# Kernel tuning notes

Measured on AMD Instinct MI355X. Metric: run time of the kernel, lower is better.

The kernel has to match this reference:

```python
import jax, jax.numpy as jnp
import numpy as np

N = 16      # manifold_dim
H = 128     # hidden_dim
B = 256     # batch
EPS = 1e-6


def setup_inputs() -> dict:
    key = jax.random.key(0)
    ks = jax.random.split(key, 14)
    def w(k, shape):
        fan_in = shape[0]
        return jax.random.uniform(k, shape, jnp.float32, -1.0, 1.0) / np.sqrt(fan_in)
    return {
        "points": jax.random.normal(ks[0], (B, N), jnp.float32),
        # metric network: N -> H -> N*N
        "mW1": w(ks[1], (N, H)), "mb1": jnp.zeros((H,), jnp.float32),
        "mW2": w(ks[2], (H, N * N)), "mb2": jnp.zeros((N * N,), jnp.float32),
        # christoffel network: 3 -> H -> 1
        "cW1": w(ks[3], (3, H)), "cb1": jnp.zeros((H,), jnp.float32),
        "cW2": w(ks[4], (H, 1)), "cb2": jnp.zeros((1,), jnp.float32),
        # ricci network: 4N -> 2H -> N*N
        "rW1": w(ks[5], (4 * N, 2 * H)), "rb1": jnp.zeros((2 * H,), jnp.float32),
        "rW2": w(ks[6], (2 * H, N * N)), "rb2": jnp.zeros((N * N,), jnp.float32),
    }


def reference(points, mW1, mb1, mW2, mb2, cW1, cb1, cW2, cb2, rW1, rb1, rW2, rb2):
    b = points.shape[0]
    n = N
    # ---- metric: (b, n, n) ----
    mh = jax.nn.relu(points @ mW1 + mb1)
    metric = (mh @ mW2 + mb2).reshape(b, n, n)
    metric = metric + EPS * jnp.eye(n, dtype=metric.dtype)
    metric = 0.5 * (metric + jnp.swapaxes(metric, -2, -1))

    # ---- christoffel: vectorized over all (i,j,k) triples ----
    # inputs per triple: [metric_ij, metric_jk, metric_ki]
    m_ij = jnp.broadcast_to(metric[:, :, :, None], (b, n, n, n))
    m_jk = jnp.broadcast_to(metric[:, None, :, :], (b, n, n, n))
    mT = jnp.swapaxes(metric, -2, -1)  # mT[b,i,k] = metric[b,k,i]
    m_ki = jnp.broadcast_to(mT[:, :, None, :], (b, n, n, n))
    ch_in = jnp.stack([m_ij, m_jk, m_ki], axis=-1)        # (b,n,n,n,3)
    ch_h = jnp.tanh(ch_in @ cW1 + cb1)                    # (b,n,n,n,H)
    christoffel = (ch_h @ cW2 + cb2)[..., 0]              # (b,n,n,n)

    # ---- ricci: vectorized over all (i,j) pairs ----
    p_b = jnp.broadcast_to(points[:, None, None, :], (b, n, n, n))
    m_i = jnp.broadcast_to(metric[:, :, None, :], (b, n, n, n))
    m_j = jnp.broadcast_to(metric[:, None, :, :], (b, n, n, n))
    r_in = jnp.concatenate([p_b, m_i, m_j, christoffel], axis=-1)  # (b,n,n,4n)
    r_h = jax.nn.relu(r_in @ rW1 + rb1)                   # (b,n,n,2H)
    r_out = (r_h @ rW2 + rb2).reshape(b, n, n, n, n)      # (b,i,j,n,n)
    r_out = 0.5 * (r_out + jnp.swapaxes(r_out, -1, -2))
    ricci = r_out.sum(axis=(1, 2)) / (n * n)              # (b,n,n)
    return ricci
```

## Files before the change

kernel.cpp:

```cpp
#include <hip/hip_runtime.h>
#include <hip/hip_bf16.h>

#define NDIM 16
#define HDIM 128
#define BATCH 256
#define EPS_D 1e-6f

typedef float v2f __attribute__((ext_vector_type(2)));
static __device__ __forceinline__ v2f v2(float a, float b) {
  v2f r; r.x = a; r.y = b; return r;
}
static __device__ __forceinline__ v2f splat(float a) {
  v2f r; r.x = a; r.y = a; return r;
}

__global__ __launch_bounds__(256) void metric_proj_kernel(
    const float* __restrict__ points,
    const float* __restrict__ mW1, const float* __restrict__ mb1,
    const float* __restrict__ mW2, const float* __restrict__ mb2,
    const float* __restrict__ rW1, const float* __restrict__ rb1,
    float* __restrict__ metric,
    float* __restrict__ A1, float* __restrict__ Mi, float* __restrict__ Mj,
    float* __restrict__ G) {
  int b = blockIdx.x;
  int t = threadIdx.x;
  __shared__ float p[16];
  __shared__ float mh[128];
  __shared__ float raw[256];
  __shared__ float M[256];
  G[b * 256 + t] = 0.f;
  if (t < 16) p[t] = points[b * 16 + t];
  __syncthreads();
  if (t < 128) {
    float acc = mb1[t];
#pragma unroll
    for (int k = 0; k < 16; ++k) acc = fmaf(p[k], mW1[k * 128 + t], acc);
    mh[t] = fmaxf(acc, 0.f);
  }
  __syncthreads();
  {
    float acc = mb2[t];
#pragma unroll 8
    for (int h = 0; h < 128; ++h) acc = fmaf(mh[h], mW2[h * 256 + t], acc);
    raw[t] = acc;
  }
  __syncthreads();
  {
    int i = t >> 4, j = t & 15;
    float v = 0.5f * (raw[i * 16 + j] + raw[j * 16 + i]);
    if (i == j) v += EPS_D;
    M[t] = v;
    metric[b * 256 + t] = v;
  }
  __syncthreads();
  {
    int h = t;
    float wB[16], wC[16];
#pragma unroll
    for (int c = 0; c < 16; ++c) {
      wB[c] = rW1[(16 + c) * 256 + h];
      wC[c] = rW1[(32 + c) * 256 + h];
    }
    float a = rb1[h];
#pragma unroll
    for (int r = 0; r < 16; ++r) a = fmaf(p[r], rW1[r * 256 + h], a);
    A1[b * 256 + h] = a;
#pragma unroll 2
    for (int i = 0; i < 16; ++i) {
      float mi = 0.f, mj = 0.f;
#pragma unroll
      for (int c = 0; c < 16; ++c) {
        float m = M[i * 16 + c];
        mi = fmaf(m, wB[c], mi);
        mj = fmaf(m, wC[c], mj);
      }
      Mi[(b * 16 + i) * 256 + h] = mi;
      Mj[(b * 16 + i) * 256 + h] = mj;
    }
  }
}

__global__ __launch_bounds__(128, 6) void chr_kernel(
    const float* __restrict__ metric,
    const float* __restrict__ cW1, const float* __restrict__ cb1,
    const float* __restrict__ cW2, const float* __restrict__ cb2,
    const float* __restrict__ rW1,
    const float* __restrict__ A1, const float* __restrict__ Mi,
    const float* __restrict__ Mj,
    float* __restrict__ G) {
  int bi = blockIdx.x;
  int b = bi >> 4, i = bi & 15;
  int t = threadIdx.x;
  int w = t >> 6, l = t & 63;
  __shared__ float M[256];
  __shared__ float4 z[128];
  __shared__ float4 w2p[32];
  __shared__ float4 ch4[64];
  float* chf = (float*)ch4;
  M[t] = metric[b * 256 + t];
  M[t + 128] = metric[b * 256 + t + 128];
  {
    const float S = 2.8853900817779268f;
    z[t] = make_float4(S * cW1[t], S * cW1[128 + t], S * cW1[256 + t],
                       S * cb1[t]);
    ((float*)w2p)[t] = cW2[t];
  }
  __syncthreads();

  {
    int jk0 = w * 128 + l, jk1 = jk0 + 64;
    int j0 = jk0 >> 4, k0 = jk0 & 15;
    int j1 = jk1 >> 4, k1 = jk1 & 15;
    v2f x0 = v2(M[i * 16 + j0], M[i * 16 + j1]);
    v2f x1 = v2(M[j0 * 16 + k0], M[j1 * 16 + k1]);
    v2f x2 = v2(M[k0 * 16 + i], M[k1 * 16 + i]);
    v2f acc = splat(cb2[0]);
    for (int hq = 0; hq < 32; ++hq) {
      float4 W2 = w2p[hq];
      float w2u[4] = {W2.x, W2.y, W2.z, W2.w};
#pragma unroll
      for (int u = 0; u < 4; ++u) {
        float4 Q = z[hq * 4 + u];
        v2f pre = __builtin_elementwise_fma(
            x0, splat(Q.x),
            __builtin_elementwise_fma(
                x1, splat(Q.y),
                __builtin_elementwise_fma(x2, splat(Q.z), splat(Q.w))));
        v2f e;
        e.x = __builtin_amdgcn_exp2f(pre.x);
        e.y = __builtin_amdgcn_exp2f(pre.y);
        v2f ep = e + splat(1.f);
        v2f r;
        r.x = __builtin_amdgcn_rcpf(ep.x);
        r.y = __builtin_amdgcn_rcpf(ep.y);
        v2f th = __builtin_elementwise_fma(splat(-2.f), r, splat(1.f));
        acc = __builtin_elementwise_fma(th, splat(w2u[u]), acc);
      }
    }
    chf[jk0] = acc.x;
    chf[jk1] = acc.y;
  }
  __syncthreads();

  {
    int h0 = w * 128 + l, h1 = h0 + 64;
    v2f rc2[16];
#pragma unroll
    for (int kk = 0; kk < 16; ++kk)
      rc2[kk] = v2(rW1[(48 + kk) * 256 + h0], rW1[(48 + kk) * 256 + h1]);
    v2f base = v2(A1[b * 256 + h0] + Mi[bi * 256 + h0],
                  A1[b * 256 + h1] + Mi[bi * 256 + h1]);
    v2f hacc = splat(0.f);
    for (int jj = 0; jj < 16; ++jj) {
      float4 c0 = ch4[jj * 4 + 0];
      float4 c1 = ch4[jj * 4 + 1];
      float4 c2v = ch4[jj * 4 + 2];
      float4 c3 = ch4[jj * 4 + 3];
      v2f mj = v2(Mj[(b * 16 + jj) * 256 + h0], Mj[(b * 16 + jj) * 256 + h1]);
      v2f cp = base + mj;
      float cc[16] = {c0.x, c0.y, c0.z, c0.w, c1.x, c1.y, c1.z, c1.w,
                      c2v.x, c2v.y, c2v.z, c2v.w, c3.x, c3.y, c3.z, c3.w};
#pragma unroll
      for (int kk = 0; kk < 16; ++kk)
        cp = __builtin_elementwise_fma(splat(cc[kk]), rc2[kk], cp);
      v2f rl;
      rl.x = fmaxf(cp.x, 0.f);
      rl.y = fmaxf(cp.y, 0.f);
      hacc += rl;
    }
    atomicAdd(&G[b * 256 + h0], hacc.x);
    atomicAdd(&G[b * 256 + h1], hacc.y);
  }
}

__global__ __launch_bounds__(256) void final_kernel(
    const float* __restrict__ G,
    const float* __restrict__ rW2, const float* __restrict__ rb2,
    float* __restrict__ out) {
  int b = blockIdx.x;
  int t = threadIdx.x;
  __shared__ float4 Gs[64];
  __shared__ float T[256];
  if (t < 64) Gs[t] = ((const float4*)(G + b * 256))[t];
  __syncthreads();
  float acc = 256.f * rb2[t];
#pragma unroll 4
  for (int h4 = 0; h4 < 64; ++h4) {
    float4 gg = Gs[h4];
    acc = fmaf(gg.x, rW2[(h4 * 4 + 0) * 256 + t], acc);
    acc = fmaf(gg.y, rW2[(h4 * 4 + 1) * 256 + t], acc);
    acc = fmaf(gg.z, rW2[(h4 * 4 + 2) * 256 + t], acc);
    acc = fmaf(gg.w, rW2[(h4 * 4 + 3) * 256 + t], acc);
  }
  T[t] = acc * (1.f / 256.f);
  __syncthreads();
  int k = t >> 4, lcol = t & 15;
  out[b * 256 + t] = 0.5f * (T[k * 16 + lcol] + T[lcol * 16 + k]);
}

extern "C" void kernel_launch(void* const* d_in, const int* in_sizes, int n_in,
                              void* d_out, int out_size, void* d_ws, size_t ws_size,
                              hipStream_t stream) {
  const float* points = (const float*)d_in[0];
  const float* mW1 = (const float*)d_in[1];
  const float* mb1 = (const float*)d_in[2];
  const float* mW2 = (const float*)d_in[3];
  const float* mb2 = (const float*)d_in[4];
  const float* cW1 = (const float*)d_in[5];
  const float* cb1 = (const float*)d_in[6];
  const float* cW2 = (const float*)d_in[7];
  const float* cb2 = (const float*)d_in[8];
  const float* rW1 = (const float*)d_in[9];
  const float* rb1 = (const float*)d_in[10];
  const float* rW2 = (const float*)d_in[11];
  const float* rb2 = (const float*)d_in[12];
  float* out = (float*)d_out;

  float* ws = (float*)d_ws;
  float* metric = ws;
  float* A1 = metric + 65536;
  float* Mi = A1 + 65536;
  float* Mj = Mi + 1048576;
  float* G = Mj + 1048576;

  metric_proj_kernel<<<BATCH, 256, 0, stream>>>(points, mW1, mb1, mW2, mb2,
                                                rW1, rb1, metric, A1, Mi, Mj, G);
  chr_kernel<<<BATCH * NDIM, 128, 0, stream>>>(metric, cW1, cb1, cW2, cb2, rW1,
                                               A1, Mi, Mj, G);
  final_kernel<<<BATCH, 256, 0, stream>>>(G, rW2, rb2, out);
}
```

Before: 135.7 us.

## Replace tanh exp/rcp with clamped rational polynomial using packed FMA

The Christoffel MLP's tanh, previously computed with exp2 and rcp per hidden unit, becomes a clamped odd rational polynomial evaluated with inline v_pk_fma/v_pk_mul asm. The two reciprocals per pair share one rcp through a product trick. The hidden dimension is now split across the two waves, each handling four (j,k) triples per thread, and partial sums are reduced through shared memory. The aim is to move work off the transcendental unit onto packed FP32 FMA throughput, at the cost of an approximation error near the clamp, extra shared memory, and one more barrier.

New measurement: 159.5 us. 1.18x slower.

```diff
diff --git a/kernel.cpp b/kernel.cpp
--- a/kernel.cpp
+++ b/kernel.cpp
@@ -13,6 +13,34 @@
 static __device__ __forceinline__ v2f splat(float a) {
   v2f r; r.x = a; r.y = a; return r;
 }
+static __device__ __forceinline__ v2f pk_fma(v2f a, v2f b, v2f c) {
+  v2f d;
+  asm("v_pk_fma_f32 %0, %1, %2, %3" : "=v"(d) : "v"(a), "v"(b), "v"(c));
+  return d;
+}
+static __device__ __forceinline__ v2f pk_mul(v2f a, v2f b) {
+  v2f d;
+  asm("v_pk_mul_f32 %0, %1, %2" : "=v"(d) : "v"(a), "v"(b));
+  return d;
+}
+static __device__ __forceinline__ v2f pk_add(v2f a, v2f b) {
+  v2f d;
+  asm("v_pk_add_f32 %0, %1, %2" : "=v"(d) : "v"(a), "v"(b));
+  return d;
+}
+
+#define TCLAMP 7.99881172180175781f
+#define CA1 4.89352455891786e-03f
+#define CA3 6.37261928875436e-04f
+#define CA5 1.48572235717979e-05f
+#define CA7 5.12229709037114e-08f
+#define CA9 -8.60467152213735e-11f
+#define CA11 2.00018790482477e-13f
+#define CA13 -2.76076847742355e-16f
+#define CB0 4.89352518554385e-03f
+#define CB2 2.26843463243900e-03f
+#define CB4 1.18534705686654e-04f
+#define CB6 1.19825839466702e-06f
 
 __global__ __launch_bounds__(256) void metric_proj_kernel(
     const float* __restrict__ points,
@@ -93,80 +121,109 @@
   int t = threadIdx.x;
   int w = t >> 6, l = t & 63;
   __shared__ float M[256];
-  __shared__ float4 z[128];
-  __shared__ float4 w2p[32];
-  __shared__ float4 ch4[64];
-  float* chf = (float*)ch4;
+  __shared__ float4 zAB[128];
+  __shared__ float4 zCD[128];
+  __shared__ float2 zE[128];
+  __shared__ float chpart[512];
+  __shared__ float2 chd[256];
   M[t] = metric[b * 256 + t];
   M[t + 128] = metric[b * 256 + t + 128];
   {
-    const float S = 2.8853900817779268f;
-    z[t] = make_float4(S * cW1[t], S * cW1[128 + t], S * cW1[256 + t],
-                       S * cb1[t]);
-    ((float*)w2p)[t] = cW2[t];
-  }
-  __syncthreads();
-
-  {
-    int jk0 = w * 128 + l, jk1 = jk0 + 64;
-    int j0 = jk0 >> 4, k0 = jk0 & 15;
-    int j1 = jk1 >> 4, k1 = jk1 & 15;
-    v2f x0 = v2(M[i * 16 + j0], M[i * 16 + j1]);
-    v2f x1 = v2(M[j0 * 16 + k0], M[j1 * 16 + k1]);
-    v2f x2 = v2(M[k0 * 16 + i], M[k1 * 16 + i]);
-    v2f acc = splat(cb2[0]);
-    for (int hq = 0; hq < 32; ++hq) {
-      float4 W2 = w2p[hq];
-      float w2u[4] = {W2.x, W2.y, W2.z, W2.w};
-#pragma unroll
-      for (int u = 0; u < 4; ++u) {
-        float4 Q = z[hq * 4 + u];
-        v2f pre = __builtin_elementwise_fma(
-            x0, splat(Q.x),
-            __builtin_elementwise_fma(
-                x1, splat(Q.y),
-                __builtin_elementwise_fma(x2, splat(Q.z), splat(Q.w))));
-        v2f e;
-        e.x = __builtin_amdgcn_exp2f(pre.x);
-        e.y = __builtin_amdgcn_exp2f(pre.y);
-        v2f ep = e + splat(1.f);
-        v2f r;
-        r.x = __builtin_amdgcn_rcpf(ep.x);
-        r.y = __builtin_amdgcn_rcpf(ep.y);
-        v2f th = __builtin_elementwise_fma(splat(-2.f), r, splat(1.f));
-        acc = __builtin_elementwise_fma(th, splat(w2u[u]), acc);
-      }
-    }
-    chf[jk0] = acc.x;
-    chf[jk1] = acc.y;
-  }
-  __syncthreads();
-
-  {
-    int h0 = w * 128 + l, h1 = h0 + 64;
+    float w0 = cW1[t], w1 = cW1[128 + t], w2b = cW1[256 + t];
+    float b1v = cb1[t], w2o = cW2[t];
+    zAB[t] = make_float4(w0, w0, w1, w1);
+    zCD[t] = make_float4(w2b, w2b, b1v, b1v);
+    zE[t] = make_float2(w2o, w2o);
+  }
+  __syncthreads();
+
+  {
+    int j0 = l >> 4, k0 = l & 15;
+    v2f x0A = v2(M[i * 16 + j0], M[i * 16 + j0 + 4]);
+    v2f x0B = v2(M[i * 16 + j0 + 8], M[i * 16 + j0 + 12]);
+    v2f x1A = v2(M[l], M[l + 64]);
+    v2f x1B = v2(M[l + 128], M[l + 192]);
+    v2f x2p = splat(M[k0 * 16 + i]);
+    v2f accA = (w == 0) ? splat(cb2[0]) : splat(0.f);
+    v2f accB = accA;
+    const v2f kA13 = splat(CA13), kA11 = splat(CA11), kA9 = splat(CA9);
+    const v2f kA7 = splat(CA7), kA5 = splat(CA5), kA3 = splat(CA3);
+    const v2f kA1 = splat(CA1);
+    const v2f kB6 = splat(CB6), kB4 = splat(CB4), kB2 = splat(CB2);
+    const v2f kB0 = splat(CB0);
+#pragma unroll 2
+    for (int hh = 0; hh < 64; ++hh) {
+      int h = (w << 6) + hh;
+      float4 ZA = zAB[h];
+      float4 ZC = zCD[h];
+      float2 ZE = zE[h];
+      v2f w0p = v2(ZA.x, ZA.y), w1p = v2(ZA.z, ZA.w);
+      v2f w2bp = v2(ZC.x, ZC.y), b1p = v2(ZC.z, ZC.w);
+      v2f w2p = v2(ZE.x, ZE.y);
+      v2f bb = pk_fma(x2p, w2bp, b1p);
+      v2f tA = pk_fma(x0A, w0p, pk_fma(x1A, w1p, bb));
+      v2f tB = pk_fma(x0B, w0p, pk_fma(x1B, w1p, bb));
+      tA.x = __builtin_amdgcn_fmed3f(tA.x, -TCLAMP, TCLAMP);
+      tA.y = __builtin_amdgcn_fmed3f(tA.y, -TCLAMP, TCLAMP);
+      tB.x = __builtin_amdgcn_fmed3f(tB.x, -TCLAMP, TCLAMP);
+      tB.y = __builtin_amdgcn_fmed3f(tB.y, -TCLAMP, TCLAMP);
+      v2f sA = pk_mul(tA, tA), sB = pk_mul(tB, tB);
+      v2f pA = pk_fma(sA, kA13, kA11), pB = pk_fma(sB, kA13, kA11);
+      pA = pk_fma(pA, sA, kA9);  pB = pk_fma(pB, sB, kA9);
+      pA = pk_fma(pA, sA, kA7);  pB = pk_fma(pB, sB, kA7);
+      pA = pk_fma(pA, sA, kA5);  pB = pk_fma(pB, sB, kA5);
+      pA = pk_fma(pA, sA, kA3);  pB = pk_fma(pB, sB, kA3);
+      pA = pk_fma(pA, sA, kA1);  pB = pk_fma(pB, sB, kA1);
+      pA = pk_mul(pA, tA);       pB = pk_mul(pB, tB);
+      v2f qA = pk_fma(sA, kB6, kB4), qB = pk_fma(sB, kB6, kB4);
+      qA = pk_fma(qA, sA, kB2);  qB = pk_fma(qB, sB, kB2);
+      qA = pk_fma(qA, sA, kB0);  qB = pk_fma(qB, sB, kB0);
+      v2f pAB = pk_mul(qA, qB);
+      float r = __builtin_amdgcn_rcpf(pAB.x * pAB.y);
+      v2f u2 = v2(r * pAB.y, r * pAB.x);
+      v2f invA = pk_mul(u2, qB);
+      v2f invB = pk_mul(u2, qA);
+      v2f thA = pk_mul(pA, invA), thB = pk_mul(pB, invB);
+      accA = pk_fma(thA, w2p, accA);
+      accB = pk_fma(thB, w2p, accB);
+    }
+    chpart[w * 256 + l] = accA.x;
+    chpart[w * 256 + l + 64] = accA.y;
+    chpart[w * 256 + l + 128] = accB.x;
+    chpart[w * 256 + l + 192] = accB.y;
+  }
+  __syncthreads();
+  {
+    float s0 = chpart[t] + chpart[256 + t];
+    float s1 = chpart[t + 128] + chpart[256 + t + 128];
+    chd[t] = make_float2(s0, s0);
+    chd[t + 128] = make_float2(s1, s1);
+  }
+  __syncthreads();
+
+  {
+    int h0 = t, h1 = t + 128;
     v2f rc2[16];
 #pragma unroll
-    for (int kk = 0; kk < 16; ++kk)
-      rc2[kk] = v2(rW1[(48 + kk) * 256 + h0], rW1[(48 + kk) * 256 + h1]);
-    v2f base = v2(A1[b * 256 + h0] + Mi[bi * 256 + h0],
-                  A1[b * 256 + h1] + Mi[bi * 256 + h1]);
+    for (int kk = 0; kk < 16; ++kk) {
+      const float* row = rW1 + (48 + kk) * 256;
+      rc2[kk] = v2(row[h0], row[h1]);
+    }
+    const float* A1b = A1 + b * 256;
+    const float* Mib = Mi + bi * 256;
+    v2f base = v2(A1b[h0] + Mib[h0], A1b[h1] + Mib[h1]);
     v2f hacc = splat(0.f);
     for (int jj = 0; jj < 16; ++jj) {
-      float4 c0 = ch4[jj * 4 + 0];
-      float4 c1 = ch4[jj * 4 + 1];
-      float4 c2v = ch4[jj * 4 + 2];
-      float4 c3 = ch4[jj * 4 + 3];
-      v2f mj = v2(Mj[(b * 16 + jj) * 256 + h0], Mj[(b * 16 + jj) * 256 + h1]);
-      v2f cp = base + mj;
-      float cc[16] = {c0.x, c0.y, c0.z, c0.w, c1.x, c1.y, c1.z, c1.w,
-                      c2v.x, c2v.y, c2v.z, c2v.w, c3.x, c3.y, c3.z, c3.w};
-#pragma unroll
-      for (int kk = 0; kk < 16; ++kk)
-        cp = __builtin_elementwise_fma(splat(cc[kk]), rc2[kk], cp);
-      v2f rl;
-      rl.x = fmaxf(cp.x, 0.f);
-      rl.y = fmaxf(cp.y, 0.f);
-      hacc += rl;
+      const float* Mjr = Mj + (b * 16 + jj) * 256;
+      v2f cp = pk_add(base, v2(Mjr[h0], Mjr[h1]));
+#pragma unroll
+      for (int kk = 0; kk < 16; ++kk) {
+        float2 c = chd[jj * 16 + kk];
+        cp = pk_fma(v2(c.x, c.y), rc2[kk], cp);
+      }
+      cp.x = fmaxf(cp.x, 0.f);
+      cp.y = fmaxf(cp.y, 0.f);
+      hacc = pk_add(hacc, cp);
     }
     atomicAdd(&G[b * 256 + h0], hacc.x);
     atomicAdd(&G[b * 256 + h1], hacc.y);
```
